# Kernel tuning notes

Measured on AMD Instinct MI355X. Metric: run time of the kernel, lower is better.

The kernel has to match this reference:

```python
import jax, jax.numpy as jnp
import numpy as np

ENT_TOTAL = 500000
REL_TOTAL = 1000
HIDDEN = 256
BATCH = 8192
NEGS = 16  # negative_ent + negative_rel
MARGIN = 1.0


def setup_inputs() -> dict:
    key = jax.random.key(0)
    ks = jax.random.split(key, 8)
    return {
        "pos_h": jax.random.randint(ks[0], (BATCH,), 0, ENT_TOTAL, dtype=jnp.int64 if jax.config.jax_enable_x64 else jnp.int32).astype(jnp.int32),
        "pos_t": jax.random.randint(ks[1], (BATCH,), 0, ENT_TOTAL).astype(jnp.int32),
        "pos_r": jax.random.randint(ks[2], (BATCH,), 0, REL_TOTAL).astype(jnp.int32),
        "neg_h": jax.random.randint(ks[3], (BATCH * NEGS,), 0, ENT_TOTAL).astype(jnp.int32),
        "neg_t": jax.random.randint(ks[4], (BATCH * NEGS,), 0, ENT_TOTAL).astype(jnp.int32),
        "neg_r": jax.random.randint(ks[5], (BATCH * NEGS,), 0, REL_TOTAL).astype(jnp.int32),
        "ent_embeddings": jax.random.normal(ks[6], (ENT_TOTAL, HIDDEN), dtype=jnp.float32) * 0.1,
        "rel_embeddings": jax.random.normal(ks[7], (REL_TOTAL, HIDDEN), dtype=jnp.float32) * 0.1,
    }


def _ccorr(a, b):
    # circular correlation via FFT: real(ifft(conj(fft(a)) * fft(b)))
    fa = jnp.fft.fft(a, axis=-1)
    fb = jnp.fft.fft(b, axis=-1)
    return jnp.fft.ifft(jnp.conj(fa) * fb, axis=-1).real.astype(a.dtype)


def _l2_normalize(x, axis=1, eps=1e-12):
    sq = jnp.sum(x * x, axis=axis, keepdims=True)
    return x * jax.lax.rsqrt(jnp.maximum(sq, eps))


def _calc(head, tail, rel):
    rel_n = _l2_normalize(rel, axis=1)
    ent = _ccorr(head, tail)
    return -jax.nn.sigmoid(jnp.sum(rel_n * ent, axis=1, keepdims=True))


def reference(pos_h, pos_t, pos_r, neg_h, neg_t, neg_r, ent_embeddings, rel_embeddings):
    ph = ent_embeddings[pos_h]
    pt = ent_embeddings[pos_t]
    pr = rel_embeddings[pos_r]
    nh = ent_embeddings[neg_h]
    nt = ent_embeddings[neg_t]
    nr = rel_embeddings[neg_r]
    p_score = _calc(ph, pt, pr).reshape(-1, 1)            # [B, 1]
    n_score = _calc(nh, nt, nr).reshape(-1, NEGS)         # [B, NEGS]
    n_score = jnp.mean(n_score, axis=1, keepdims=True)    # [B, 1]
    loss = jnp.sum(jnp.maximum(p_score - n_score + MARGIN, 0.0))
    return loss
```

## Files before the change

### kernel.cpp

```cpp
#include <hip/hip_runtime.h>
#include <math.h>

#define HIDDEN 256
#define BATCH 8192
#define NEGS 16
#define NSCORES (BATCH + BATCH * NEGS)
#define PI2 6.28318530717958647692f

typedef unsigned int uint32;
typedef _Float16 h2v __attribute__((ext_vector_type(2)));

__device__ __forceinline__ float2 cmul(float2 a, float2 b) {
    return make_float2(fmaf(a.x, b.x, -a.y * b.y), fmaf(a.x, b.y, a.y * b.x));
}
__device__ __forceinline__ float2 cmulc(float2 a, float cx, float cy) {
    return make_float2(fmaf(a.x, cx, -a.y * cy), fmaf(a.x, cy, a.y * cx));
}
__device__ __forceinline__ float2 mulnegi(float2 a) { return make_float2(a.y, -a.x); }

__device__ __forceinline__ uint32 pk(float a, float b) {
    auto p = __builtin_amdgcn_cvt_pkrtz(a, b);
    uint32 u; __builtin_memcpy(&u, &p, 4);
    return u;
}
__device__ __forceinline__ float2 unpk(uint32 u) {
    h2v h; __builtin_memcpy(&h, &u, 4);
    return make_float2((float)h.x, (float)h.y);
}

template<int C>
__device__ __forceinline__ float fdpp(float v) {
    return __uint_as_float((unsigned)__builtin_amdgcn_mov_dpp(
        (int)__float_as_uint(v), C, 0xf, 0xf, true));
}
template<int IMM>
__device__ __forceinline__ float fswz(float v) {
    return __uint_as_float((unsigned)__builtin_amdgcn_ds_swizzle(
        (int)__float_as_uint(v), IMM));
}

__device__ __forceinline__ void bfly4(float2 a, float2 b, float2 c, float2 d,
                                      float2& u0, float2& u1, float2& u2, float2& u3) {
    float2 apc = make_float2(a.x + c.x, a.y + c.y);
    float2 amc = make_float2(a.x - c.x, a.y - c.y);
    float2 bpd = make_float2(b.x + d.x, b.y + d.y);
    float2 bmd = make_float2(b.x - d.x, b.y - d.y);
    u0 = make_float2(apc.x + bpd.x, apc.y + bpd.y);
    u2 = make_float2(apc.x - bpd.x, apc.y - bpd.y);
    u1 = make_float2(amc.x + bmd.y, amc.y - bmd.x);
    u3 = make_float2(amc.x - bmd.y, amc.y + bmd.x);
}

__device__ __forceinline__ void fft16(float2 z[16]) {
    const float R  = 0.70710678118654752440f;
    const float C1 = 0.92387953251128675613f;
    const float S1 = 0.38268343236508977173f;
    #pragma unroll
    for (int p = 0; p < 4; ++p) {
        float2 u0, u1, u2, u3;
        bfly4(z[p], z[p+4], z[p+8], z[p+12], u0, u1, u2, u3);
        z[p] = u0; z[p+4] = u1; z[p+8] = u2; z[p+12] = u3;
    }
    z[5]  = cmulc(z[5],  C1, -S1);
    z[6]  = cmulc(z[6],  R,  -R );
    z[7]  = cmulc(z[7],  S1, -C1);
    z[9]  = cmulc(z[9],  R,  -R );
    z[10] = mulnegi(z[10]);
    z[11] = cmulc(z[11], -R, -R );
    z[13] = cmulc(z[13], S1, -C1);
    z[14] = cmulc(z[14], -R, -R );
    z[15] = cmulc(z[15], -C1, S1);
    float2 o[16];
    #pragma unroll
    for (int k = 0; k < 4; ++k) {
        float2 v0, v1, v2, v3;
        bfly4(z[4*k], z[4*k+1], z[4*k+2], z[4*k+3], v0, v1, v2, v3);
        o[k] = v0; o[k+4] = v1; o[k+8] = v2; o[k+12] = v3;
    }
    #pragma unroll
    for (int i = 0; i < 16; ++i) z[i] = o[i];
}

__device__ __forceinline__ void twiddle256(float2 z[16], int L) {
    float s1, c1, s4, c4;
    __sincosf(-PI2 * (1.0f / 256.0f) * (float)L, &s1, &c1);
    __sincosf(-PI2 * (4.0f / 256.0f) * (float)L, &s4, &c4);
    const float2 w1 = make_float2(c1, s1);
    const float2 w4 = make_float2(c4, s4);
    const float2 w2 = cmul(w1, w1);
    const float2 w3 = cmul(w2, w1);
    const float2 w8 = cmul(w4, w4);
    const float2 w12 = cmul(w8, w4);
    float2 wp[16];
    wp[1] = w1; wp[2] = w2; wp[3] = w3;
    wp[4] = w4; wp[5] = cmul(w4, w1); wp[6] = cmul(w4, w2); wp[7] = cmul(w4, w3);
    wp[8] = w8; wp[9] = cmul(w8, w1); wp[10] = cmul(w8, w2); wp[11] = cmul(w8, w3);
    wp[12] = w12; wp[13] = cmul(w12, w1); wp[14] = cmul(w12, w2); wp[15] = cmul(w12, w3);
    #pragma unroll
    for (int f1 = 1; f1 < 16; ++f1) z[f1] = cmul(z[f1], wp[f1]);
}

__device__ __forceinline__ int sigmap(int L) {
    return (L == 0) ? 0 : (L == 15 ? 8 : (L < 8 ? L : L + 1));
}

#define RRS 18
#define RGS (16 * RRS + 2)

__global__ __launch_bounds__(256) void rel_fft_kernel(
    const float* __restrict__ rel, float2* __restrict__ FrP)
{
    __shared__ __align__(16) float2 Tr[16 * RGS];
    const int tid = threadIdx.x;
    const int gb = tid >> 4;
    const int L = tid & 15;
    const int ri = blockIdx.x * 16 + gb;
    if (ri >= 1000) return;

    const float* __restrict__ rrow = rel + (long)ri * HIDDEN;
    float2 z[16];
    float rn2 = 0.f;
    #pragma unroll
    for (int n1 = 0; n1 < 16; ++n1) {
        const float v = rrow[16 * n1 + L];
        z[n1] = make_float2(v, 0.f);
        rn2 = fmaf(v, v, rn2);
    }
    rn2 += fdpp<0xB1>(rn2);
    rn2 += fdpp<0x4E>(rn2);
    rn2 += fswz<0x101F>(rn2);
    rn2 += fswz<0x201F>(rn2);
    const float s = rsqrtf(fmaxf(rn2, 1e-12f)) * (1.0f / 256.0f);

    fft16(z);
    twiddle256(z, L);

    float2* __restrict__ Tg = Tr + gb * RGS;
    {
        float4* __restrict__ wp4 = (float4*)(Tg + L * RRS);
        #pragma unroll
        for (int j = 0; j < 8; ++j)
            wp4[j] = make_float4(z[2*j].x, z[2*j].y, z[2*j+1].x, z[2*j+1].y);
    }
    const int sig = sigmap(L);
    __builtin_amdgcn_wave_barrier();
    #pragma unroll
    for (int n2 = 0; n2 < 16; ++n2) z[n2] = Tg[n2 * RRS + sig];

    fft16(z);

    float2* __restrict__ ob = FrP + (long)ri * 256 + sig;
    #pragma unroll
    for (int f2 = 0; f2 < 16; ++f2)
        ob[16 * f2] = make_float2(z[f2].x * (s * 0.5f), z[f2].y * (s * 0.25f));
}

#define RSU 20
#define GSU (16 * RSU + 4)

__global__ __launch_bounds__(256, 5) void score_kernel(
    const int* __restrict__ pos_h, const int* __restrict__ pos_t, const int* __restrict__ pos_r,
    const int* __restrict__ neg_h, const int* __restrict__ neg_t, const int* __restrict__ neg_r,
    const float* __restrict__ ent, const float2* __restrict__ FrP,
    float* __restrict__ scores)
{
    __shared__ __align__(16) uint32 Tu[16 * GSU];
    const int tid = threadIdx.x;
    const int gb = tid >> 4;
    const int L = tid & 15;
    const int s = blockIdx.x * 16 + gb;

    const bool isp = s < BATCH;
    const int jj = isp ? s : s - BATCH;
    const int hi = (isp ? pos_h : neg_h)[jj];
    const int ti = (isp ? pos_t : neg_t)[jj];
    const int ri = (isp ? pos_r : neg_r)[jj];

    const float* __restrict__ hrow = ent + (long)hi * HIDDEN;
    const float* __restrict__ trow = ent + (long)ti * HIDDEN;

    float2 z[16];
    #pragma unroll
    for (int n1 = 0; n1 < 16; ++n1)
        z[n1] = make_float2(hrow[16 * n1 + L], trow[16 * n1 + L]);

    fft16(z);
    twiddle256(z, L);

    uint32* __restrict__ Tg = Tu + gb * GSU;
    {
        uint4* __restrict__ wp4 = (uint4*)(Tg + L * RSU);
        #pragma unroll
        for (int j = 0; j < 4; ++j)
            wp4[j] = make_uint4(pk(z[4*j].x,   z[4*j].y),
                                pk(z[4*j+1].x, z[4*j+1].y),
                                pk(z[4*j+2].x, z[4*j+2].y),
                                pk(z[4*j+3].x, z[4*j+3].y));
    }

    const int sig = sigmap(L);
    const float2* __restrict__ fb = FrP + (long)ri * 256 + sig;

    float2 fr0[8];
    #pragma unroll
    for (int f2 = 0; f2 < 8; ++f2) fr0[f2] = fb[16 * f2];

    __builtin_amdgcn_wave_barrier();
    #pragma unroll
    for (int n2 = 0; n2 < 16; ++n2) z[n2] = unpk(Tg[n2 * RSU + sig]);

    fft16(z);

    float2 fr1[8];
    #pragma unroll
    for (int f2 = 0; f2 < 8; ++f2) fr1[f2] = fb[16 * (f2 + 8)];

    const bool isL0 = (L == 0), isL15 = (L == 15);
    float S = 0.f;
    #pragma unroll
    for (int f2 = 0; f2 < 16; ++f2) {
        float2 src = z[15 - f2];
        float2 Bm = make_float2(fdpp<0x140>(src.x), fdpp<0x140>(src.y));
        float2 own0 = z[(16 - f2) & 15];
        float2 B;
        B.x = isL0 ? own0.x : (isL15 ? src.x : Bm.x);
        B.y = isL0 ? own0.y : (isL15 ? src.y : Bm.y);
        const float2 A = z[f2];
        const float2 fr = (f2 < 8) ? fr0[f2 & 7] : fr1[f2 & 7];
        const float imAB = A.x * B.y + A.y * B.x;
        const float dmag = (B.x * B.x + B.y * B.y) - (A.x * A.x + A.y * A.y);
        S = fmaf(fr.x, imAB, fmaf(fr.y, dmag, S));
    }

    S += fdpp<0xB1>(S);
    S += fdpp<0x4E>(S);
    S += fswz<0x101F>(S);
    S += fswz<0x201F>(S);

    if (L == 0) scores[s] = -1.0f / (1.0f + __expf(-S));
}

__global__ __launch_bounds__(256) void loss1_kernel(
    const float* __restrict__ scores, float* __restrict__ partial)
{
    __shared__ float red[4];
    const int b = blockIdx.x * 256 + threadIdx.x;
    const float p = scores[b];
    const float* __restrict__ np = scores + BATCH + b * NEGS;
    float n = 0.f;
    #pragma unroll
    for (int j = 0; j < NEGS; ++j) n += np[j];
    n *= (1.0f / NEGS);
    float v = fmaxf(p - n + 1.0f, 0.0f);
    #pragma unroll
    for (int m = 32; m >= 1; m >>= 1) v += __shfl_xor(v, m);
    const int wave = threadIdx.x >> 6, lane = threadIdx.x & 63;
    if (lane == 0) red[wave] = v;
    __syncthreads();
    if (threadIdx.x == 0)
        partial[blockIdx.x] = (red[0] + red[1]) + (red[2] + red[3]);
}

__global__ __launch_bounds__(64) void loss2_kernel(
    const float* __restrict__ partial, float* __restrict__ out)
{
    const int lane = threadIdx.x;
    float v = (lane < 32) ? partial[lane] : 0.f;
    #pragma unroll
    for (int m = 32; m >= 1; m >>= 1) v += __shfl_xor(v, m);
    if (lane == 0) out[0] = v;
}

extern "C" void kernel_launch(void* const* d_in, const int* in_sizes, int n_in,
                              void* d_out, int out_size, void* d_ws, size_t ws_size,
                              hipStream_t stream) {
    (void)in_sizes; (void)n_in; (void)out_size; (void)ws_size;
    const int* pos_h = (const int*)d_in[0];
    const int* pos_t = (const int*)d_in[1];
    const int* pos_r = (const int*)d_in[2];
    const int* neg_h = (const int*)d_in[3];
    const int* neg_t = (const int*)d_in[4];
    const int* neg_r = (const int*)d_in[5];
    const float* ent = (const float*)d_in[6];
    const float* rel = (const float*)d_in[7];

    float2* FrP = (float2*)d_ws;
    float* scores = (float*)((char*)d_ws + 1000 * 256 * sizeof(float2));
    float* partial = scores + NSCORES;
    float* out = (float*)d_out;

    rel_fft_kernel<<<dim3(63), dim3(256), 0, stream>>>(rel, FrP);
    score_kernel<<<dim3(NSCORES / 16), dim3(256), 0, stream>>>(
        pos_h, pos_t, pos_r, neg_h, neg_t, neg_r, ent, FrP, scores);
    loss1_kernel<<<dim3(BATCH / 256), dim3(256), 0, stream>>>(scores, partial);
    loss2_kernel<<<dim3(1), dim3(64), 0, stream>>>(partial, out);
}
```

Before: 68.00 us.

## Use Hermitian symmetry of relation spectrum to halve frequency reduction loop

```diff
diff --git a/kernel.cpp b/kernel.cpp
--- a/kernel.cpp
+++ b/kernel.cpp
@@ -6,6 +6,7 @@
 #define NEGS 16
 #define NSCORES (BATCH + BATCH * NEGS)
 #define PI2 6.28318530717958647692f
+#define FR_STRIDE 136
 
 typedef unsigned int uint32;
 typedef _Float16 h2v __attribute__((ext_vector_type(2)));
@@ -84,20 +85,21 @@
 __device__ __forceinline__ void twiddle256(float2 z[16], int L) {
     float s1, c1, s4, c4;
     __sincosf(-PI2 * (1.0f / 256.0f) * (float)L, &s1, &c1);
-    __sincosf(-PI2 * (4.0f / 256.0f) * (float)L, &s4, &c4);
+    __sincosf(-PI2 * (1.0f / 64.0f) * (float)L, &s4, &c4);
     const float2 w1 = make_float2(c1, s1);
     const float2 w4 = make_float2(c4, s4);
     const float2 w2 = cmul(w1, w1);
     const float2 w3 = cmul(w2, w1);
-    const float2 w8 = cmul(w4, w4);
-    const float2 w12 = cmul(w8, w4);
-    float2 wp[16];
-    wp[1] = w1; wp[2] = w2; wp[3] = w3;
-    wp[4] = w4; wp[5] = cmul(w4, w1); wp[6] = cmul(w4, w2); wp[7] = cmul(w4, w3);
-    wp[8] = w8; wp[9] = cmul(w8, w1); wp[10] = cmul(w8, w2); wp[11] = cmul(w8, w3);
-    wp[12] = w12; wp[13] = cmul(w12, w1); wp[14] = cmul(w12, w2); wp[15] = cmul(w12, w3);
-    #pragma unroll
-    for (int f1 = 1; f1 < 16; ++f1) z[f1] = cmul(z[f1], wp[f1]);
+    z[1] = cmul(z[1], w1); z[2] = cmul(z[2], w2); z[3] = cmul(z[3], w3);
+    float2 m = w4;
+    #pragma unroll
+    for (int a = 1; a < 4; ++a) {
+        z[4*a]   = cmul(z[4*a], m);
+        z[4*a+1] = cmul(cmul(z[4*a+1], m), w1);
+        z[4*a+2] = cmul(cmul(z[4*a+2], m), w2);
+        z[4*a+3] = cmul(cmul(z[4*a+3], m), w3);
+        if (a < 3) m = cmul(m, w4);
+    }
 }
 
 __device__ __forceinline__ int sigmap(int L) {
@@ -108,7 +110,7 @@
 #define RGS (16 * RRS + 2)
 
 __global__ __launch_bounds__(256) void rel_fft_kernel(
-    const float* __restrict__ rel, float2* __restrict__ FrP)
+    const float* __restrict__ rel, float2* __restrict__ FrH)
 {
     __shared__ __align__(16) float2 Tr[16 * RGS];
     const int tid = threadIdx.x;
@@ -149,19 +151,25 @@
 
     fft16(z);
 
-    float2* __restrict__ ob = FrP + (long)ri * 256 + sig;
-    #pragma unroll
-    for (int f2 = 0; f2 < 16; ++f2)
-        ob[16 * f2] = make_float2(z[f2].x * (s * 0.5f), z[f2].y * (s * 0.25f));
+    float2* __restrict__ ob = FrH + (long)ri * FR_STRIDE + sig;
+    #pragma unroll
+    for (int f2 = 0; f2 < 8; ++f2) {
+        float cx = s * z[f2].x;
+        float cy = 0.5f * s * z[f2].y;
+        if (sig == 0 && f2 == 0) { cx *= 0.5f; cy = 0.f; }
+        ob[16 * f2] = make_float2(cx, cy);
+    }
+    if (L == 0)
+        FrH[(long)ri * FR_STRIDE + 128] = make_float2(0.5f * s * z[8].x, 0.f);
 }
 
 #define RSU 20
 #define GSU (16 * RSU + 4)
 
-__global__ __launch_bounds__(256, 5) void score_kernel(
+__global__ __launch_bounds__(256, 6) void score_kernel(
     const int* __restrict__ pos_h, const int* __restrict__ pos_t, const int* __restrict__ pos_r,
     const int* __restrict__ neg_h, const int* __restrict__ neg_t, const int* __restrict__ neg_r,
-    const float* __restrict__ ent, const float2* __restrict__ FrP,
+    const float* __restrict__ ent, const float2* __restrict__ FrH,
     float* __restrict__ scores)
 {
     __shared__ __align__(16) uint32 Tu[16 * GSU];
@@ -199,11 +207,6 @@
     }
 
     const int sig = sigmap(L);
-    const float2* __restrict__ fb = FrP + (long)ri * 256 + sig;
-
-    float2 fr0[8];
-    #pragma unroll
-    for (int f2 = 0; f2 < 8; ++f2) fr0[f2] = fb[16 * f2];
 
     __builtin_amdgcn_wave_barrier();
     #pragma unroll
@@ -211,14 +214,16 @@
 
     fft16(z);
 
-    float2 fr1[8];
-    #pragma unroll
-    for (int f2 = 0; f2 < 8; ++f2) fr1[f2] = fb[16 * (f2 + 8)];
+    const float2* __restrict__ fb = FrH + (long)ri * FR_STRIDE + sig;
+    float2 fr[8];
+    #pragma unroll
+    for (int f2 = 0; f2 < 8; ++f2) fr[f2] = fb[16 * f2];
+    const float2 c128 = FrH[(long)ri * FR_STRIDE + 128];
 
     const bool isL0 = (L == 0), isL15 = (L == 15);
     float S = 0.f;
     #pragma unroll
-    for (int f2 = 0; f2 < 16; ++f2) {
+    for (int f2 = 0; f2 < 8; ++f2) {
         float2 src = z[15 - f2];
         float2 Bm = make_float2(fdpp<0x140>(src.x), fdpp<0x140>(src.y));
         float2 own0 = z[(16 - f2) & 15];
@@ -226,11 +231,11 @@
         B.x = isL0 ? own0.x : (isL15 ? src.x : Bm.x);
         B.y = isL0 ? own0.y : (isL15 ? src.y : Bm.y);
         const float2 A = z[f2];
-        const float2 fr = (f2 < 8) ? fr0[f2 & 7] : fr1[f2 & 7];
         const float imAB = A.x * B.y + A.y * B.x;
         const float dmag = (B.x * B.x + B.y * B.y) - (A.x * A.x + A.y * A.y);
-        S = fmaf(fr.x, imAB, fmaf(fr.y, dmag, S));
-    }
+        S = fmaf(fr[f2].x, imAB, fmaf(fr[f2].y, dmag, S));
+    }
+    if (isL0) S = fmaf(c128.x, 2.f * z[8].x * z[8].y, S);
 
     S += fdpp<0xB1>(S);
     S += fdpp<0x4E>(S);
@@ -284,14 +289,14 @@
     const float* ent = (const float*)d_in[6];
     const float* rel = (const float*)d_in[7];
 
-    float2* FrP = (float2*)d_ws;
-    float* scores = (float*)((char*)d_ws + 1000 * 256 * sizeof(float2));
+    float2* FrH = (float2*)d_ws;
+    float* scores = (float*)((char*)d_ws + 1000 * FR_STRIDE * sizeof(float2));
     float* partial = scores + NSCORES;
     float* out = (float*)d_out;
 
-    rel_fft_kernel<<<dim3(63), dim3(256), 0, stream>>>(rel, FrP);
+    rel_fft_kernel<<<dim3(63), dim3(256), 0, stream>>>(rel, FrH);
     score_kernel<<<dim3(NSCORES / 16), dim3(256), 0, stream>>>(
-        pos_h, pos_t, pos_r, neg_h, neg_t, neg_r, ent, FrP, scores);
+        pos_h, pos_t, pos_r, neg_h, neg_t, neg_r, ent, FrH, scores);
     loss1_kernel<<<dim3(BATCH / 256), dim3(256), 0, stream>>>(scores, partial);
     loss2_kernel<<<dim3(1), dim3(64), 0, stream>>>(partial, out);
 }
```

Measured after the change: 62.89 us. 7.5% less time.
